# Optimization experiments

Measured on AMD Instinct MI355X. Metric: run time of the kernel, lower is better.

The kernel has to match this reference:

```python
import jax, jax.numpy as jnp
import numpy as np

N, C = 50000, 91
K_PRE = 1000            # pre-NMS top-k candidates (fixed shape for jit)
DET_PER_IMG = 100
SCORE_THRESH = 0.05
NMS_THRESH = 0.5
MIN_SIZE = 0.01
LOG_SCALE_CLAMP = float(np.log(1000.0 / 16.0))  # torchvision BoxCoder clamp
BBOX_W = (10.0, 10.0, 5.0, 5.0)


def setup_inputs() -> dict:
    key = jax.random.key(0)
    k1, k2, k3, k4, k5, k6 = jax.random.split(key, 6)
    class_logits = jax.random.normal(k1, (N, C), jnp.float32) * 2.0
    box_regression = jax.random.normal(k2, (N, C * 4), jnp.float32) * 0.5
    x1 = jax.random.uniform(k3, (N,), jnp.float32) * 1200.0
    y1 = jax.random.uniform(k4, (N,), jnp.float32) * 700.0
    w = jax.random.uniform(k5, (N,), jnp.float32) * 150.0 + 4.0
    h = jax.random.uniform(k6, (N,), jnp.float32) * 150.0 + 4.0
    proposals = jnp.stack([x1, y1, x1 + w, y1 + h], axis=1)
    return {"class_logits": class_logits, "box_regression": box_regression,
            "proposals": proposals, "image_h": 800, "image_w": 1333}


def _decode(rel, props):
    # torchvision BoxCoder.decode_single with weights (10,10,5,5)
    wx, wy, ww, wh = BBOX_W
    pw = props[:, 2] - props[:, 0]
    ph = props[:, 3] - props[:, 1]
    cx = props[:, 0] + 0.5 * pw
    cy = props[:, 1] + 0.5 * ph
    dx = rel[:, 0] / wx
    dy = rel[:, 1] / wy
    dw = jnp.minimum(rel[:, 2] / ww, LOG_SCALE_CLAMP)
    dh = jnp.minimum(rel[:, 3] / wh, LOG_SCALE_CLAMP)
    pcx = dx * pw + cx
    pcy = dy * ph + cy
    ppw = jnp.exp(dw) * pw
    pph = jnp.exp(dh) * ph
    return jnp.stack([pcx - 0.5 * ppw, pcy - 0.5 * pph,
                      pcx + 0.5 * ppw, pcy + 0.5 * pph], axis=1)


def _iou_matrix(b):
    # b: [K,4] -> [K,K] pairwise IoU
    area = jnp.maximum(b[:, 2] - b[:, 0], 0.0) * jnp.maximum(b[:, 3] - b[:, 1], 0.0)
    lt = jnp.maximum(b[:, None, :2], b[None, :, :2])
    rb = jnp.minimum(b[:, None, 2:], b[None, :, 2:])
    wh = jnp.maximum(rb - lt, 0.0)
    inter = wh[..., 0] * wh[..., 1]
    return inter / (area[:, None] + area[None, :] - inter + 1e-7)


def _postprocess(class_logits, box_regression, proposals, image_h, image_w):
    num_classes = class_logits.shape[-1]
    n = proposals.shape[0]
    props = jnp.broadcast_to(proposals[:, None, :], (n, num_classes, 4)).reshape(-1, 4)
    boxes = _decode(box_regression.reshape(-1, 4), props)       # [N*C, 4]
    # clip_boxes_to_image
    boxes = jnp.stack([
        jnp.clip(boxes[:, 0], 0.0, float(image_w)),
        jnp.clip(boxes[:, 1], 0.0, float(image_h)),
        jnp.clip(boxes[:, 2], 0.0, float(image_w)),
        jnp.clip(boxes[:, 3], 0.0, float(image_h)),
    ], axis=1)
    scores = jax.nn.softmax(class_logits, axis=-1)               # [N, C]
    # drop background class 0
    boxes = boxes.reshape(n, num_classes, 4)[:, 1:].reshape(-1, 4)    # [N*(C-1), 4]
    scores = scores[:, 1:].reshape(-1)                                # [N*(C-1)]
    labels = jnp.broadcast_to(jnp.arange(1, num_classes), (n, num_classes - 1)).reshape(-1)
    # score threshold + remove small boxes -> mask (fixed-shape)
    w = boxes[:, 2] - boxes[:, 0]
    h = boxes[:, 3] - boxes[:, 1]
    valid = (scores > SCORE_THRESH) & (w >= MIN_SIZE) & (h >= MIN_SIZE)
    masked_scores = jnp.where(valid, scores, -1.0)
    s_k, idx = jax.lax.top_k(masked_scores, K_PRE)               # pre-NMS candidates
    b_k = boxes[idx]
    l_k = labels[idx]
    keep0 = s_k > 0.0
    # batched NMS via per-class coordinate offset
    offset = l_k.astype(b_k.dtype) * float(image_w + image_h + 2)
    iou = _iou_matrix(b_k + offset[:, None])                     # [K,K]
    ar = jnp.arange(K_PRE)
    def body(i, keep):
        sup = keep[i] & (iou[i] > NMS_THRESH) & (ar > i)
        return keep & ~sup
    keep = jax.lax.fori_loop(0, K_PRE, body, keep0)
    final_scores = jnp.where(keep, s_k, -1.0)
    s_out, j = jax.lax.top_k(final_scores, DET_PER_IMG)
    ok = s_out > 0.0
    boxes_out = jnp.where(ok[:, None], b_k[j], 0.0)
    scores_out = jnp.where(ok, s_out, 0.0)
    labels_out = jnp.where(ok, l_k[j], 0)
    return boxes_out, scores_out, labels_out


def reference(class_logits, box_regression, proposals, image_h, image_w):
    return _postprocess(class_logits, box_regression, proposals, image_h, image_w)
```

## Files before the change

kernel.cpp:

```cpp
#include <hip/hip_runtime.h>
#include <cstdint>

#define NROWS 50000
#define NCLS  91
#define KPRE  1000
#define NDET  100
#define CAP   4096
#define NBINS 512
#define BIN_OFF 7680u
#define LOGCLAMP 4.135166556742356f
#define ROWS_PER_BLOCK 16
#define PBLK 3126
#define PB   3126
#define GCHUNK 128

constexpr size_t OFF_CNT     = 0;
constexpr size_t OFF_ROWMAX  = 64;
constexpr size_t OFF_COMPACT = 100096;
constexpr size_t OFF_SSCORE  = 132864;
constexpr size_t OFF_SGIDX   = 136960;
constexpr size_t OFF_SLABEL  = 141056;
constexpr size_t OFF_BRAW    = 145152;
constexpr size_t OFF_BNMS    = 161536;
constexpr size_t OFF_MASK    = 177920;
constexpr size_t OFF_PARTIAL = 305920;
constexpr size_t OFF_HIST512 = 3506944;

__device__ __forceinline__ bool decode_box(int row, int c,
    const float* __restrict__ regr, const float* __restrict__ props,
    float W, float H, float4& b) {
  const float4 rr = *reinterpret_cast<const float4*>(regr + (size_t)row * (NCLS * 4) + c * 4);
  const float4 pp = *reinterpret_cast<const float4*>(props + (size_t)row * 4);
  float pw = pp.z - pp.x, ph = pp.w - pp.y;
  float cx = pp.x + 0.5f * pw, cy = pp.y + 0.5f * ph;
  float dx = rr.x / 10.0f, dy = rr.y / 10.0f;
  float dw = fminf(rr.z / 5.0f, LOGCLAMP);
  float dh = fminf(rr.w / 5.0f, LOGCLAMP);
  float pcx = dx * pw + cx, pcy = dy * ph + cy;
  float ppw = expf(dw) * pw, pph = expf(dh) * ph;
  float x1 = fminf(fmaxf(pcx - 0.5f * ppw, 0.f), W);
  float y1 = fminf(fmaxf(pcy - 0.5f * pph, 0.f), H);
  float x2 = fminf(fmaxf(pcx + 0.5f * ppw, 0.f), W);
  float y2 = fminf(fmaxf(pcy + 0.5f * pph, 0.f), H);
  b = make_float4(x1, y1, x2, y2);
  return (x2 - x1 >= 0.01f) && (y2 - y1 >= 0.01f);
}

__global__ __launch_bounds__(256)
void pass1_kernel(const float* __restrict__ logits,
                  const float* __restrict__ regr,
                  const float* __restrict__ props,
                  const int* __restrict__ p_imh,
                  const int* __restrict__ p_imw,
                  uint16_t* __restrict__ partial,
                  uint16_t* __restrict__ rowmax) {
  __shared__ uint32_t hist[NBINS];
  const int t = threadIdx.x;
  hist[t] = 0;
  hist[t + 256] = 0;
  __syncthreads();

  const int sub = t & 15;
  const int grp = t >> 4;
  const int row = blockIdx.x * ROWS_PER_BLOCK + grp;
  if (row < NROWS) {
    const float W = (float)(*p_imw), H = (float)(*p_imh);
    const float* lr = logits + (size_t)row * NCLS;
    float x[6];
    #pragma unroll
    for (int j = 0; j < 6; ++j) {
      int c = sub + 16 * j;
      x[j] = (c < NCLS) ? lr[c] : -INFINITY;
    }
    float m = x[0];
    #pragma unroll
    for (int j = 1; j < 6; ++j) m = fmaxf(m, x[j]);
    m = fmaxf(m, __shfl_xor(m, 1));
    m = fmaxf(m, __shfl_xor(m, 2));
    m = fmaxf(m, __shfl_xor(m, 4));
    m = fmaxf(m, __shfl_xor(m, 8));
    float e[6]; float s = 0.f;
    #pragma unroll
    for (int j = 0; j < 6; ++j) {
      e[j] = (sub + 16 * j < NCLS) ? expf(x[j] - m) : 0.f;
      s += e[j];
    }
    s += __shfl_xor(s, 1);
    s += __shfl_xor(s, 2);
    s += __shfl_xor(s, 4);
    s += __shfl_xor(s, 8);

    int maxbin = 0;
    #pragma unroll
    for (int j = 0; j < 6; ++j) {
      int c = sub + 16 * j;
      if (c >= 1 && c < NCLS) {
        float score = e[j] / s;
        if (score > 0.05f) {
          float4 b;
          if (decode_box(row, c, regr, props, W, H, b)) {
            uint32_t bin = (__float_as_uint(score) >> 17) - BIN_OFF;
            atomicAdd(&hist[bin], 1u);
            if ((int)bin > maxbin) maxbin = (int)bin;
          }
        }
      }
    }
    maxbin = max(maxbin, __shfl_xor(maxbin, 1));
    maxbin = max(maxbin, __shfl_xor(maxbin, 2));
    maxbin = max(maxbin, __shfl_xor(maxbin, 4));
    maxbin = max(maxbin, __shfl_xor(maxbin, 8));
    if (sub == 0) rowmax[row] = (uint16_t)maxbin;
  }
  __syncthreads();
  const int blk = blockIdx.x;
  uint32_t v0 = hist[t], v1 = hist[t + 256];
  partial[(size_t)t * PB + blk]         = (uint16_t)(v0 > 65535u ? 65535u : v0);
  partial[(size_t)(t + 256) * PB + blk] = (uint16_t)(v1 > 65535u ? 65535u : v1);
}

__global__ __launch_bounds__(64)
void binsum_kernel(const uint16_t* __restrict__ partial, uint32_t* __restrict__ hist512) {
  const int b = blockIdx.x;
  const uint32_t* r32 = reinterpret_cast<const uint32_t*>(partial + (size_t)b * PB);
  uint32_t s = 0;
  for (int k = threadIdx.x; k < PB / 2; k += 64) {
    uint32_t v = r32[k];
    s += (v & 0xffffu) + (v >> 16);
  }
  #pragma unroll
  for (int off = 32; off; off >>= 1) s += __shfl_xor(s, off);
  if (threadIdx.x == 0) hist512[b] = s;
}

__global__ __launch_bounds__(512)
void scan_kernel(const uint32_t* __restrict__ hist512, uint32_t* __restrict__ cnt) {
  __shared__ uint32_t sh[NBINS];
  const int t = threadIdx.x;
  if (t == 0) cnt[1] = 0;
  uint32_t s = hist512[t];
  sh[t] = s;
  __syncthreads();
  uint32_t v = s;
  for (int off = 1; off < NBINS; off <<= 1) {
    uint32_t add = (t + off < NBINS) ? sh[t + off] : 0;
    __syncthreads();
    v += add;
    sh[t] = v;
    __syncthreads();
  }
  const uint32_t total = sh[0];
  if (total == 0) { if (t == 0) cnt[0] = 0xFFFFFFFFu; return; }
  const uint32_t target = total < (uint32_t)KPRE ? total : (uint32_t)KPRE;
  const uint32_t rs_t = sh[t];
  const uint32_t rs_n = (t < NBINS - 1) ? sh[t + 1] : 0;
  if (rs_t >= target && rs_n < target) cnt[0] = (uint32_t)t;
}

__global__ __launch_bounds__(256)
void refine_kernel(const float* __restrict__ logits,
                   const float* __restrict__ regr,
                   const float* __restrict__ props,
                   const int* __restrict__ p_imh,
                   const int* __restrict__ p_imw,
                   const uint16_t* __restrict__ rowmax,
                   uint32_t* __restrict__ cnt,
                   unsigned long long* __restrict__ compact) {
  const int t = threadIdx.x;
  const int lane = t & 63;
  const int g = lane >> 4;
  const int sub = lane & 15;
  const uint32_t cut = cnt[0];
  const int myrow0 = blockIdx.x * 256 + t;
  bool qual = (myrow0 < NROWS) && ((uint32_t)rowmax[myrow0] >= cut);
  unsigned long long bm = __ballot(qual);
  if (!bm) return;
  const int waveBase = blockIdx.x * 256 + (t & ~63);
  const float W = (float)(*p_imw), H = (float)(*p_imh);

  while (bm) {
    int bsel[4];
    #pragma unroll
    for (int k = 0; k < 4; ++k) {
      bsel[k] = bm ? (__ffsll((unsigned long long)bm) - 1) : -1;
      if (bm) bm &= bm - 1;
    }
    const int myb = bsel[g];
    const int row = waveBase + (myb >= 0 ? myb : 0);
    const float* lr = logits + (size_t)row * NCLS;

    float x[6];
    #pragma unroll
    for (int j = 0; j < 6; ++j) {
      int c = sub + 16 * j;
      x[j] = (c < NCLS) ? lr[c] : -INFINITY;
    }
    float m = x[0];
    #pragma unroll
    for (int j = 1; j < 6; ++j) m = fmaxf(m, x[j]);
    m = fmaxf(m, __shfl_xor(m, 1));
    m = fmaxf(m, __shfl_xor(m, 2));
    m = fmaxf(m, __shfl_xor(m, 4));
    m = fmaxf(m, __shfl_xor(m, 8));
    float e[6]; float s = 0.f;
    #pragma unroll
    for (int j = 0; j < 6; ++j) {
      e[j] = (sub + 16 * j < NCLS) ? expf(x[j] - m) : 0.f;
      s += e[j];
    }
    s += __shfl_xor(s, 1);
    s += __shfl_xor(s, 2);
    s += __shfl_xor(s, 4);
    s += __shfl_xor(s, 8);

    if (myb >= 0) {
      #pragma unroll
      for (int j = 0; j < 6; ++j) {
        int c = sub + 16 * j;
        if (c >= 1 && c < NCLS) {
          float score = e[j] / s;
          if (score > 0.05f) {
            float4 bb;
            if (decode_box(row, c, regr, props, W, H, bb)) {
              uint32_t bits = __float_as_uint(score);
              uint32_t bin = (bits >> 17) - BIN_OFF;
              if (bin >= cut) {
                uint32_t pos = atomicAdd(&cnt[1], 1u);
                if (pos < CAP) {
                  uint32_t gidx = (uint32_t)row * 90u + (uint32_t)(c - 1);
                  compact[pos] = ((unsigned long long)bits << 32) |
                                 (unsigned long long)(0xFFFFFFFFu - gidx);
                }
              }
            }
          }
        }
      }
    }
  }
}

__global__ __launch_bounds__(1024)
void sort_prep_kernel(const unsigned long long* __restrict__ compact,
                      const uint32_t* __restrict__ cnt,
                      const float* __restrict__ regr, const float* __restrict__ props,
                      const int* __restrict__ p_imh, const int* __restrict__ p_imw,
                      float* __restrict__ sel_score, uint32_t* __restrict__ sel_gidx,
                      int* __restrict__ slabel, float4* __restrict__ braw,
                      float4* __restrict__ bnms) {
  __shared__ unsigned long long arr[CAP];
  const int t = threadIdx.x;
  const uint32_t M = cnt[1] < (uint32_t)CAP ? cnt[1] : (uint32_t)CAP;
  int P = 1024;
  while (P < (int)M) P <<= 1;
  for (int i = t; i < P; i += 1024) arr[i] = (i < (int)M) ? compact[i] : 0ull;
  __syncthreads();
  for (int k = 2; k <= P; k <<= 1) {
    for (int j = k >> 1; j > 0; j >>= 1) {
      for (int i = t; i < P; i += 1024) {
        int l = i ^ j;
        if (l > i) {
          unsigned long long A = arr[i], B = arr[l];
          bool up = ((i & k) == 0);
          if (up ? (A > B) : (A < B)) { arr[i] = B; arr[l] = A; }
        }
      }
      __syncthreads();
    }
  }
  if (t < KPRE) {
    unsigned long long en = arr[P - 1 - t];
    float sc; uint32_t g;
    if (en) { sc = __uint_as_float((uint32_t)(en >> 32)); g = 0xFFFFFFFFu - (uint32_t)en; }
    else    { sc = -1.f; g = 0xFFFFFFFFu; }
    sel_score[t] = sc;
    sel_gidx[t] = g;
    if (sc > 0.f) {
      int row = (int)(g / 90u);
      int c   = (int)(g % 90u) + 1;
      float W = (float)(*p_imw), H = (float)(*p_imh);
      float4 b;
      decode_box(row, c, regr, props, W, H, b);
      braw[t] = b;
      float offv = (float)c * (float)(*p_imw + *p_imh + 2);
      bnms[t] = make_float4(b.x + offv, b.y + offv, b.z + offv, b.w + offv);
      slabel[t] = c;
    } else {
      braw[t] = make_float4(0, 0, 0, 0);
      bnms[t] = make_float4(0, 0, 0, 0);
      slabel[t] = 0;
    }
  }
}

__global__ __launch_bounds__(256)
void iou_kernel(const float4* __restrict__ bnms, unsigned long long* __restrict__ mask) {
  const int i = blockIdx.x;
  const int lane = threadIdx.x & 63;
  const int wv = threadIdx.x >> 6;
  const float4 bi = bnms[i];
  const float areai = fmaxf(bi.z - bi.x, 0.f) * fmaxf(bi.w - bi.y, 0.f);
  #pragma unroll
  for (int ww = 0; ww < 4; ++ww) {
    int wd = wv * 4 + ww;
    int j = wd * 64 + lane;
    bool bit = false;
    if (j < KPRE && j > i) {
      float4 bj = bnms[j];
      float areaj = fmaxf(bj.z - bj.x, 0.f) * fmaxf(bj.w - bj.y, 0.f);
      float ltx = fmaxf(bi.x, bj.x), lty = fmaxf(bi.y, bj.y);
      float rbx = fminf(bi.z, bj.z), rby = fminf(bi.w, bj.w);
      float iw = fmaxf(rbx - ltx, 0.f), ih = fmaxf(rby - lty, 0.f);
      float inter = iw * ih;
      float iou = inter / (areai + areaj - inter + 1e-7f);
      bit = iou > 0.5f;
    }
    unsigned long long mword = __ballot(bit);
    if (lane == 0) mask[(size_t)i * 16 + wd] = mword;
  }
}

__global__ __launch_bounds__(256)
void greedy_kernel(const unsigned long long* __restrict__ mask,
                   const float* __restrict__ sel_score,
                   const int* __restrict__ slabel,
                   const float4* __restrict__ braw,
                   float* __restrict__ out) {
  __shared__ ulonglong2 buf[2][GCHUNK * 8];
  __shared__ int kept[NDET];
  __shared__ int s_done;
  const int t = threadIdx.x;
  const int lane = t & 63;
  const int wv = t >> 6;
  const ulonglong2* gm2 = reinterpret_cast<const ulonglong2*>(mask);
  constexpr int NCHUNK = (KPRE + GCHUNK - 1) / GCHUNK;

  unsigned long long kw = 0ull;
  #pragma unroll
  for (int w = 0; w < 16; ++w) {
    int j = w * 64 + lane;
    bool b = (j < KPRE) && (sel_score[j] > 0.f);
    unsigned long long mword = __ballot(b);
    if (lane == w) kw = mword;
  }
  if (t == 0) s_done = 0;

  {
    int rows = (KPRE < GCHUNK) ? KPRE : GCHUNK;
    int n2 = rows * 8;
    for (int k = t; k < n2; k += 256) buf[0][k] = gm2[k];
  }
  __syncthreads();

  int kc = 0;
  for (int c = 0; c < NCHUNK; ++c) {
    if (wv > 0 && c + 1 < NCHUNK) {
      int rows = KPRE - (c + 1) * GCHUNK;
      if (rows > GCHUNK) rows = GCHUNK;
      int n2 = rows * 8;
      size_t gbase = (size_t)(c + 1) * GCHUNK * 8;
      for (int k = t - 64; k < n2; k += 192) buf[(c + 1) & 1][k] = gm2[gbase + k];
    }
    if (wv == 0) {
      const unsigned long long* bb =
          reinterpret_cast<const unsigned long long*>(buf[c & 1]);
      int rows = KPRE - c * GCHUNK;
      if (rows > GCHUNK) rows = GCHUNK;
      unsigned long long curm = (lane < 16) ? bb[lane] : 0ull;
      for (int r = 0; r < rows; ++r) {
        unsigned long long nxt =
            (lane < 16 && r + 1 < rows) ? bb[(r + 1) * 16 + lane] : 0ull;
        int i = c * GCHUNK + r;
        unsigned long long kwv = __shfl(kw, i >> 6);
        if ((kwv >> (i & 63)) & 1ull) {
          if (lane == 0) kept[kc] = i;
          kw &= ~curm;
          ++kc;
          if (kc >= NDET) { if (lane == 0) s_done = 1; break; }
        }
        curm = nxt;
      }
    }
    __syncthreads();
    if (s_done) break;
  }

  if (wv == 0) {
    for (int q = lane; q < NDET; q += 64) {
      if (q < kc) {
        int i = kept[q];
        float4 b = braw[i];
        out[q * 4 + 0] = b.x; out[q * 4 + 1] = b.y;
        out[q * 4 + 2] = b.z; out[q * 4 + 3] = b.w;
        out[4 * NDET + q] = sel_score[i];
        out[5 * NDET + q] = (float)slabel[i];
      } else {
        out[q * 4 + 0] = 0.f; out[q * 4 + 1] = 0.f;
        out[q * 4 + 2] = 0.f; out[q * 4 + 3] = 0.f;
        out[4 * NDET + q] = 0.f;
        out[5 * NDET + q] = 0.f;
      }
    }
  }
}

extern "C" void kernel_launch(void* const* d_in, const int* in_sizes, int n_in,
                              void* d_out, int out_size, void* d_ws, size_t ws_size,
                              hipStream_t stream) {
  const float* logits = (const float*)d_in[0];
  const float* regr   = (const float*)d_in[1];
  const float* props  = (const float*)d_in[2];
  const int*   p_imh  = (const int*)d_in[3];
  const int*   p_imw  = (const int*)d_in[4];
  float* out = (float*)d_out;

  uint8_t* ws = (uint8_t*)d_ws;
  uint32_t* cnt  = (uint32_t*)(ws + OFF_CNT);
  uint16_t* rowmax = (uint16_t*)(ws + OFF_ROWMAX);
  unsigned long long* compact = (unsigned long long*)(ws + OFF_COMPACT);
  float*    sel_score = (float*)(ws + OFF_SSCORE);
  uint32_t* sel_gidx  = (uint32_t*)(ws + OFF_SGIDX);
  int*      slabel    = (int*)(ws + OFF_SLABEL);
  float4*   braw      = (float4*)(ws + OFF_BRAW);
  float4*   bnms      = (float4*)(ws + OFF_BNMS);
  unsigned long long* mask = (unsigned long long*)(ws + OFF_MASK);
  uint16_t* partial   = (uint16_t*)(ws + OFF_PARTIAL);
  uint32_t* hist512   = (uint32_t*)(ws + OFF_HIST512);


  pass1_kernel<<<PBLK, 256, 0, stream>>>(
      logits, regr, props, p_imh, p_imw, partial, rowmax);
  binsum_kernel<<<NBINS, 64, 0, stream>>>(partial, hist512);
  scan_kernel<<<1, NBINS, 0, stream>>>(hist512, cnt);
  refine_kernel<<<(NROWS + 255) / 256, 256, 0, stream>>>(
      logits, regr, props, p_imh, p_imw, rowmax, cnt, compact);
  sort_prep_kernel<<<1, 1024, 0, stream>>>(compact, cnt, regr, props, p_imh, p_imw,
                                           sel_score, sel_gidx, slabel, braw, bnms);
  iou_kernel<<<KPRE, 256, 0, stream>>>(bnms, mask);
  greedy_kernel<<<1, 256, 0, stream>>>(mask, sel_score, slabel, braw, out);
}
```

Before: 96.24 us.

## Build threshold histogram from per-row max bins in one fused scan kernel

Drops the per-block candidate histograms and the binsum pass. The score threshold is now found from a histogram of each row's maximum score bin, built inside the single-block scan kernel from the rowmax array. Counting rows instead of candidates gives a bound that stays conservative, so the threshold bin may be lower and more candidates can flow into refinement and compaction. This removes a kernel launch, a large partial-histogram write and read, and the shared atomics in pass1. The cost is more serial work in a one-block kernel and a risk of crowding the fixed-capacity compact buffer.

```diff
diff --git a/kernel.cpp b/kernel.cpp
--- a/kernel.cpp
+++ b/kernel.cpp
@@ -10,8 +10,7 @@
 #define BIN_OFF 7680u
 #define LOGCLAMP 4.135166556742356f
 #define ROWS_PER_BLOCK 16
-#define PBLK 3126
-#define PB   3126
+#define P1BLK 3125
 #define GCHUNK 128
 
 constexpr size_t OFF_CNT     = 0;
@@ -23,8 +22,6 @@
 constexpr size_t OFF_BRAW    = 145152;
 constexpr size_t OFF_BNMS    = 161536;
 constexpr size_t OFF_MASK    = 177920;
-constexpr size_t OFF_PARTIAL = 305920;
-constexpr size_t OFF_HIST512 = 3506944;
 
 __device__ __forceinline__ bool decode_box(int row, int c,
     const float* __restrict__ regr, const float* __restrict__ props,
@@ -52,96 +49,75 @@
                   const float* __restrict__ props,
                   const int* __restrict__ p_imh,
                   const int* __restrict__ p_imw,
-                  uint16_t* __restrict__ partial,
                   uint16_t* __restrict__ rowmax) {
-  __shared__ uint32_t hist[NBINS];
-  const int t = threadIdx.x;
-  hist[t] = 0;
-  hist[t + 256] = 0;
-  __syncthreads();
-
-  const int sub = t & 15;
-  const int grp = t >> 4;
-  const int row = blockIdx.x * ROWS_PER_BLOCK + grp;
-  if (row < NROWS) {
-    const float W = (float)(*p_imw), H = (float)(*p_imh);
-    const float* lr = logits + (size_t)row * NCLS;
-    float x[6];
-    #pragma unroll
-    for (int j = 0; j < 6; ++j) {
-      int c = sub + 16 * j;
-      x[j] = (c < NCLS) ? lr[c] : -INFINITY;
-    }
-    float m = x[0];
-    #pragma unroll
-    for (int j = 1; j < 6; ++j) m = fmaxf(m, x[j]);
-    m = fmaxf(m, __shfl_xor(m, 1));
-    m = fmaxf(m, __shfl_xor(m, 2));
-    m = fmaxf(m, __shfl_xor(m, 4));
-    m = fmaxf(m, __shfl_xor(m, 8));
-    float e[6]; float s = 0.f;
-    #pragma unroll
-    for (int j = 0; j < 6; ++j) {
-      e[j] = (sub + 16 * j < NCLS) ? expf(x[j] - m) : 0.f;
-      s += e[j];
-    }
-    s += __shfl_xor(s, 1);
-    s += __shfl_xor(s, 2);
-    s += __shfl_xor(s, 4);
-    s += __shfl_xor(s, 8);
-
-    int maxbin = 0;
-    #pragma unroll
-    for (int j = 0; j < 6; ++j) {
-      int c = sub + 16 * j;
-      if (c >= 1 && c < NCLS) {
-        float score = e[j] / s;
-        if (score > 0.05f) {
-          float4 b;
-          if (decode_box(row, c, regr, props, W, H, b)) {
-            uint32_t bin = (__float_as_uint(score) >> 17) - BIN_OFF;
-            atomicAdd(&hist[bin], 1u);
-            if ((int)bin > maxbin) maxbin = (int)bin;
-          }
+  const int gt  = blockIdx.x * 256 + threadIdx.x;
+  const int row = gt >> 4;
+  const int sub = gt & 15;
+  const float* lr = logits + (size_t)row * NCLS;
+
+  float x[6];
+  #pragma unroll
+  for (int j = 0; j < 6; ++j) {
+    int c = sub + 16 * j;
+    x[j] = (c < NCLS) ? lr[c] : -INFINITY;
+  }
+  float m = x[0];
+  #pragma unroll
+  for (int j = 1; j < 6; ++j) m = fmaxf(m, x[j]);
+  m = fmaxf(m, __shfl_xor(m, 1));
+  m = fmaxf(m, __shfl_xor(m, 2));
+  m = fmaxf(m, __shfl_xor(m, 4));
+  m = fmaxf(m, __shfl_xor(m, 8));
+  float e[6]; float s = 0.f;
+  #pragma unroll
+  for (int j = 0; j < 6; ++j) {
+    e[j] = (sub + 16 * j < NCLS) ? expf(x[j] - m) : 0.f;
+    s += e[j];
+  }
+  s += __shfl_xor(s, 1);
+  s += __shfl_xor(s, 2);
+  s += __shfl_xor(s, 4);
+  s += __shfl_xor(s, 8);
+
+  const float W = (float)(*p_imw), H = (float)(*p_imh);
+  int maxbin = 0;
+  #pragma unroll
+  for (int j = 0; j < 6; ++j) {
+    int c = sub + 16 * j;
+    if (c >= 1 && c < NCLS) {
+      float score = e[j] / s;
+      if (score > 0.05f) {
+        float4 b;
+        if (decode_box(row, c, regr, props, W, H, b)) {
+          uint32_t bin = (__float_as_uint(score) >> 17) - BIN_OFF;
+          if ((int)bin > maxbin) maxbin = (int)bin;
         }
       }
     }
-    maxbin = max(maxbin, __shfl_xor(maxbin, 1));
-    maxbin = max(maxbin, __shfl_xor(maxbin, 2));
-    maxbin = max(maxbin, __shfl_xor(maxbin, 4));
-    maxbin = max(maxbin, __shfl_xor(maxbin, 8));
-    if (sub == 0) rowmax[row] = (uint16_t)maxbin;
-  }
-  __syncthreads();
-  const int blk = blockIdx.x;
-  uint32_t v0 = hist[t], v1 = hist[t + 256];
-  partial[(size_t)t * PB + blk]         = (uint16_t)(v0 > 65535u ? 65535u : v0);
-  partial[(size_t)(t + 256) * PB + blk] = (uint16_t)(v1 > 65535u ? 65535u : v1);
-}
-
-__global__ __launch_bounds__(64)
-void binsum_kernel(const uint16_t* __restrict__ partial, uint32_t* __restrict__ hist512) {
-  const int b = blockIdx.x;
-  const uint32_t* r32 = reinterpret_cast<const uint32_t*>(partial + (size_t)b * PB);
-  uint32_t s = 0;
-  for (int k = threadIdx.x; k < PB / 2; k += 64) {
-    uint32_t v = r32[k];
-    s += (v & 0xffffu) + (v >> 16);
-  }
-  #pragma unroll
-  for (int off = 32; off; off >>= 1) s += __shfl_xor(s, off);
-  if (threadIdx.x == 0) hist512[b] = s;
+  }
+  maxbin = max(maxbin, __shfl_xor(maxbin, 1));
+  maxbin = max(maxbin, __shfl_xor(maxbin, 2));
+  maxbin = max(maxbin, __shfl_xor(maxbin, 4));
+  maxbin = max(maxbin, __shfl_xor(maxbin, 8));
+  if (sub == 0) rowmax[row] = (uint16_t)maxbin;
 }
 
 __global__ __launch_bounds__(512)
-void scan_kernel(const uint32_t* __restrict__ hist512, uint32_t* __restrict__ cnt) {
+void histscan_kernel(const uint16_t* __restrict__ rowmax, uint32_t* __restrict__ cnt) {
   __shared__ uint32_t sh[NBINS];
   const int t = threadIdx.x;
+  sh[t] = 0;
   if (t == 0) cnt[1] = 0;
-  uint32_t s = hist512[t];
-  sh[t] = s;
   __syncthreads();
-  uint32_t v = s;
+  const uint32_t* r32 = reinterpret_cast<const uint32_t*>(rowmax);
+  for (int k = t; k < NROWS / 2; k += 512) {
+    uint32_t v = r32[k];
+    uint32_t a = v & 0xffffu, b = v >> 16;
+    if (a) atomicAdd(&sh[a], 1u);
+    if (b) atomicAdd(&sh[b], 1u);
+  }
+  __syncthreads();
+  uint32_t v = sh[t];
   for (int off = 1; off < NBINS; off <<= 1) {
     uint32_t add = (t + off < NBINS) ? sh[t + off] : 0;
     __syncthreads();
@@ -424,14 +400,10 @@
   float4*   braw      = (float4*)(ws + OFF_BRAW);
   float4*   bnms      = (float4*)(ws + OFF_BNMS);
   unsigned long long* mask = (unsigned long long*)(ws + OFF_MASK);
-  uint16_t* partial   = (uint16_t*)(ws + OFF_PARTIAL);
-  uint32_t* hist512   = (uint32_t*)(ws + OFF_HIST512);
-
-
-  pass1_kernel<<<PBLK, 256, 0, stream>>>(
-      logits, regr, props, p_imh, p_imw, partial, rowmax);
-  binsum_kernel<<<NBINS, 64, 0, stream>>>(partial, hist512);
-  scan_kernel<<<1, NBINS, 0, stream>>>(hist512, cnt);
+
+  pass1_kernel<<<P1BLK, 256, 0, stream>>>(
+      logits, regr, props, p_imh, p_imw, rowmax);
+  histscan_kernel<<<1, NBINS, 0, stream>>>(rowmax, cnt);
   refine_kernel<<<(NROWS + 255) / 256, 256, 0, stream>>>(
       logits, regr, props, p_imh, p_imw, rowmax, cnt, compact);
   sort_prep_kernel<<<1, 1024, 0, stream>>>(compact, cnt, regr, props, p_imh, p_imw,
```

Result: slower. 101.0 us (+4.9%).
